# Kernel tuning notes

Hardware: AMD Instinct MI355X
Metric: run time of the kernel (lower is better)

Reference implementation:

```python
import jax, jax.numpy as jnp
import numpy as np

NEG_SLOPE = 0.01  # torch.nn.LeakyReLU default


def setup_inputs() -> dict:
    key = jax.random.key(0)
    ks = jax.random.split(key, 9)
    N_W, N_I, E = 100000, 100000, 2000000
    C_IN, C_OUT, N_CLS = 256, 64, 10
    sc_in = 1.0 / np.sqrt(C_IN)
    sc_cat = 1.0 / np.sqrt(2 * C_OUT)
    return {
        "x_worker": jax.random.normal(ks[0], (N_W, C_IN), dtype=jnp.float32),
        "x_item": jax.random.normal(ks[1], (N_I, C_IN), dtype=jnp.float32),
        "edge_index": jax.random.randint(ks[2], (2, E), 0, N_W, dtype=jnp.int32),
        "W_worker": jax.random.uniform(ks[3], (C_IN, C_OUT), jnp.float32, -sc_in, sc_in),
        "b_worker": jax.random.uniform(ks[4], (C_OUT,), jnp.float32, -sc_in, sc_in),
        "W_item": jax.random.uniform(ks[5], (C_IN, C_OUT), jnp.float32, -sc_in, sc_in),
        "b_item": jax.random.uniform(ks[6], (C_OUT,), jnp.float32, -sc_in, sc_in),
        "W_edge": jax.random.uniform(ks[7], (2 * C_OUT, N_CLS), jnp.float32, -sc_cat, sc_cat),
        "b_edge": jax.random.uniform(ks[8], (N_CLS,), jnp.float32, -sc_cat, sc_cat),
    }


def reference(x_worker, x_item, edge_index, W_worker, b_worker, W_item, b_item, W_edge, b_edge):
    # encoders: Linear + LeakyReLU  -> [N, C_OUT]
    xw = jax.nn.leaky_relu(x_worker @ W_worker + b_worker, NEG_SLOPE)
    xi = jax.nn.leaky_relu(x_item @ W_item + b_item, NEG_SLOPE)
    # gather endpoints per edge and concat -> [E, 2*C_OUT]
    x_cat = jnp.concatenate([xw[edge_index[0]], xi[edge_index[1]]], axis=-1)
    logits = x_cat @ W_edge + b_edge  # [E, num_class]
    return xw, xi, jax.nn.log_softmax(logits, axis=-1)
```

## Files before the change

kernel.cpp:

```cpp
#include <hip/hip_runtime.h>
#include <hip/hip_bf16.h>

#define LOG2E 1.4426950408889634f
#define LN2   0.6931471805599453f

typedef __attribute__((ext_vector_type(8))) short bf16x8;
typedef __attribute__((ext_vector_type(4))) float f32x4;

static __device__ __forceinline__ short f2bf(float f) {
  __hip_bfloat16 h = __float2bfloat16(f);
  return *reinterpret_cast<short*>(&h);
}

static __device__ __forceinline__ void gll16(const float* gsrc, float* ldst) {
  __builtin_amdgcn_global_load_lds(
      (const __attribute__((address_space(1))) void*)gsrc,
      (__attribute__((address_space(3))) void*)ldst, 16, 0, 0);
}

__global__ __launch_bounds__(256) void wprep_kernel(
    const float* __restrict__ Ww, const float* __restrict__ Wi,
    ushort* __restrict__ wfrag)
{
  int id = blockIdx.x * 256 + threadIdx.x;
  if (id >= 4096) return;
  int enc  = id >> 11;
  int f    = (id >> 6) & 31;
  int l    = id & 63;
  int nsub = f >> 3, ks = f & 7;
  const float* __restrict__ W = enc ? Wi : Ww;
  int n  = nsub * 16 + (l & 15);
  int k0 = ks * 32 + (l >> 4) * 8;
  ushort* dst = wfrag + ((size_t)(enc * 32 + f) * 64 + l) * 8;
#pragma unroll
  for (int j = 0; j < 8; ++j)
    dst[j] = (ushort)f2bf(W[(size_t)(k0 + j) * 64 + n]);
}

__global__ __launch_bounds__(256, 2) void enc_mfma4_kernel(
    const float* __restrict__ x0, const float* __restrict__ b0,
    const float* __restrict__ x1, const float* __restrict__ b1,
    const ushort* __restrict__ wfrag, float* __restrict__ out, int M)
{
  __shared__ ushort sfrag[16384];
  __shared__ float  xbuf[2][4096];

  const int enc = blockIdx.y;
  const float* __restrict__ x   = enc ? x1 : x0;
  const float* __restrict__ bia = enc ? b1 : b0;
  float* __restrict__ o = out + (size_t)enc * (size_t)M * 64u;

  const int lane = threadIdx.x & 63;
  const int wid  = threadIdx.x >> 6;
  const int rsel = lane & 15;
  const int kgrp = lane >> 4;
  const int sw   = rsel & 7;

  const int nstrips = (M + 15) >> 4;
  const int bx = blockIdx.x, G = gridDim.x;

  {
    const f32x4* src = (const f32x4*)wfrag + (size_t)enc * 2048;
    f32x4* dst = (f32x4*)sfrag;
#pragma unroll
    for (int i = 0; i < 8; ++i)
      dst[threadIdx.x + 256 * i] = src[threadIdx.x + 256 * i];
  }
  __syncthreads();

  const int niter = (bx < nstrips) ? ((nstrips - 1 - bx) / G + 1) : 0;
  if (niter == 0) return;

  const float bv = bia[wid * 16 + rsel];

  auto stage = [&](int s, int buf) {
#pragma unroll
    for (int j = 0; j < 4; ++j) {
      int R = wid * 4 + j;
      int rg = s * 16 + R; if (rg >= M) rg = M - 1;
      const float* gs = x + (size_t)rg * 256u + ((lane ^ (R & 7)) << 2);
      gll16(gs, &xbuf[buf][R * 256]);
    }
  };

  stage(bx, 0);
  if (niter > 1) {
    stage(bx + G, 1);
    asm volatile("s_waitcnt vmcnt(4)" ::: "memory");
  } else {
    asm volatile("s_waitcnt vmcnt(0)" ::: "memory");
  }
  __builtin_amdgcn_sched_barrier(0);

  for (int i = 0; i < niter; ++i) {
    const int s = bx + i * G;
    if (i) {
      if (i == niter - 1) asm volatile("s_waitcnt vmcnt(4)" ::: "memory");
      else                asm volatile("s_waitcnt vmcnt(8)" ::: "memory");
      __builtin_amdgcn_sched_barrier(0);
    }
    __builtin_amdgcn_s_barrier();
    __builtin_amdgcn_sched_barrier(0);

    const float* xb = xbuf[i & 1];

    bf16x8 a[8];
#pragma unroll
    for (int ks = 0; ks < 8; ++ks) {
      int c0 = ks * 8 + kgrp * 2;
      f32x4 lo = *(const f32x4*)&xb[rsel * 256 + (((c0    ) ^ sw) << 2)];
      f32x4 hi = *(const f32x4*)&xb[rsel * 256 + (((c0 + 1) ^ sw) << 2)];
      a[ks][0] = f2bf(lo.x); a[ks][1] = f2bf(lo.y);
      a[ks][2] = f2bf(lo.z); a[ks][3] = f2bf(lo.w);
      a[ks][4] = f2bf(hi.x); a[ks][5] = f2bf(hi.y);
      a[ks][6] = f2bf(hi.z); a[ks][7] = f2bf(hi.w);
    }

    asm volatile("s_waitcnt lgkmcnt(0)" ::: "memory");
    __builtin_amdgcn_sched_barrier(0);
    __builtin_amdgcn_s_barrier();
    __builtin_amdgcn_sched_barrier(0);

    if (i + 2 < niter) stage(bx + (i + 2) * G, i & 1);

    f32x4 acc = f32x4{0.f, 0.f, 0.f, 0.f};
#pragma unroll
    for (int ks = 0; ks < 8; ++ks) {
      bf16x8 bfr = *(const bf16x8*)(sfrag + ((size_t)((wid * 8 + ks) * 64 + lane)) * 8);
      acc = __builtin_amdgcn_mfma_f32_16x16x32_bf16(a[ks], bfr, acc, 0, 0, 0);
    }

    const int crow = s * 16 + kgrp * 4;
#pragma unroll
    for (int r = 0; r < 4; ++r) {
      int rr = crow + r;
      if (rr < M) {
        float v = acc[r] + bv;
        v = fmaxf(v, 0.01f * v);
        o[(size_t)rr * 64u + wid * 16 + rsel] = v;
      }
    }
  }
}

__global__ __launch_bounds__(256) void proj_kernel(
    const float* __restrict__ feats, const float* __restrict__ W_edge,
    const float* __restrict__ b_edge, float* __restrict__ ws, int M)
{
  const int enc = blockIdx.y;
  int row = blockIdx.x * 256 + threadIdx.x;
  if (row >= M) return;
  const float4* __restrict__ f4 =
      (const float4*)(feats + ((size_t)enc * M + row) * 64u);
  const float* __restrict__ W2 = W_edge + enc * 640;

  float acc[10];
#pragma unroll
  for (int k = 0; k < 10; ++k) acc[k] = enc ? 0.f : b_edge[k];

#pragma unroll 4
  for (int n4 = 0; n4 < 16; ++n4) {
    float4 xv = f4[n4];
    const float* w = W2 + n4 * 40;
#pragma unroll
    for (int k = 0; k < 10; ++k) acc[k] = fmaf(xv.x, w[k],      acc[k]);
#pragma unroll
    for (int k = 0; k < 10; ++k) acc[k] = fmaf(xv.y, w[10 + k], acc[k]);
#pragma unroll
    for (int k = 0; k < 10; ++k) acc[k] = fmaf(xv.z, w[20 + k], acc[k]);
#pragma unroll
    for (int k = 0; k < 10; ++k) acc[k] = fmaf(xv.w, w[30 + k], acc[k]);
  }

  float* orow = ws + ((size_t)enc * M + row) * 16u;
#pragma unroll
  for (int k = 0; k < 10; ++k) orow[k] = acc[k];
}

__global__ __launch_bounds__(256) void edge_kernel(
    const int* __restrict__ ei, const float* __restrict__ ws,
    float* __restrict__ out, int E, int M)
{
  __shared__ float sm[2560];
  long e = (long)blockIdx.x * 256 + threadIdx.x;
  float l[10];
#pragma unroll
  for (int k = 0; k < 10; ++k) l[k] = 0.f;

  if (e < E) {
    int e0 = ei[e];
    int e1 = ei[E + e];
    const float4* pw = (const float4*)ws + (size_t)e0 * 4u;
    const float4* pi = (const float4*)ws + ((size_t)M + e1) * 4u;
    float4 a0 = pw[0], a1 = pw[1], a2 = pw[2];
    float4 c0 = pi[0], c1 = pi[1], c2 = pi[2];
    l[0] = a0.x + c0.x; l[1] = a0.y + c0.y; l[2] = a0.z + c0.z; l[3] = a0.w + c0.w;
    l[4] = a1.x + c1.x; l[5] = a1.y + c1.y; l[6] = a1.z + c1.z; l[7] = a1.w + c1.w;
    l[8] = a2.x + c2.x; l[9] = a2.y + c2.y;
    float m = l[0];
#pragma unroll
    for (int k = 1; k < 10; ++k) m = fmaxf(m, l[k]);
    float s = 0.f;
#pragma unroll
    for (int k = 0; k < 10; ++k) { l[k] = (l[k] - m) * LOG2E; s += exp2f(l[k]); }
    float ls = log2f(s);
#pragma unroll
    for (int k = 0; k < 10; ++k) l[k] = (l[k] - ls) * LN2;
  }

#pragma unroll
  for (int k = 0; k < 10; ++k) sm[threadIdx.x * 10 + k] = l[k];
  __syncthreads();
  const f32x4* sm4 = (const f32x4*)sm;
  f32x4* ob = (f32x4*)(out + (size_t)blockIdx.x * 2560u);
  long lim4 = ((long)E * 10) >> 2;
  long base4 = (long)blockIdx.x * 640;
#pragma unroll
  for (int j = 0; j < 3; ++j) {
    int idx = j * 256 + threadIdx.x;
    if (idx < 640 && base4 + idx < lim4) ob[idx] = sm4[idx];
  }
}

__global__ __launch_bounds__(256) void enc_kernel_f32(
    const float* __restrict__ x0, const float* __restrict__ W0, const float* __restrict__ b0,
    const float* __restrict__ x1, const float* __restrict__ W1, const float* __restrict__ b1,
    float* __restrict__ out, int M)
{
  const int enc = blockIdx.y;
  const float* __restrict__ x = enc ? x1 : x0;
  const float* __restrict__ W = enc ? W1 : W0;
  const float* __restrict__ b = enc ? b1 : b0;
  float* __restrict__ o = out + (size_t)enc * (size_t)M * 64u;

  const int lane = threadIdx.x & 63;
  const int wid  = threadIdx.x >> 6;
  int row0 = __builtin_amdgcn_readfirstlane(blockIdx.x * 64 + wid * 16);
  const float* __restrict__ xrow = x + (size_t)row0 * 256u;

  float acc[16];
#pragma unroll
  for (int r = 0; r < 16; ++r) acc[r] = 0.f;

  if (row0 + 16 <= M) {
#pragma unroll 4
    for (int k = 0; k < 256; ++k) {
      float wv = W[k * 64 + lane];
#pragma unroll
      for (int r = 0; r < 16; ++r)
        acc[r] = fmaf(xrow[r * 256 + k], wv, acc[r]);
    }
    float bias = b[lane];
#pragma unroll
    for (int r = 0; r < 16; ++r) {
      float v = acc[r] + bias;
      v = fmaxf(v, 0.01f * v);
      o[(size_t)(row0 + r) * 64u + lane] = v;
    }
  } else if (row0 < M) {
    int nr = M - row0;
    for (int k = 0; k < 256; ++k) {
      float wv = W[k * 64 + lane];
      for (int r = 0; r < nr; ++r)
        acc[r] = fmaf(xrow[r * 256 + k], wv, acc[r]);
    }
    float bias = b[lane];
    for (int r = 0; r < nr; ++r) {
      float v = acc[r] + bias;
      v = fmaxf(v, 0.01f * v);
      o[(size_t)(row0 + r) * 64u + lane] = v;
    }
  }
}

__global__ __launch_bounds__(256) void edge_kernel_direct(
    const int* __restrict__ ei, const float* __restrict__ feats,
    const float* __restrict__ W_edge, const float* __restrict__ b_edge,
    float* __restrict__ out, int E, int M)
{
  __shared__ float sm[2560];
  long e = (long)blockIdx.x * 256 + threadIdx.x;
  float l[10];
#pragma unroll
  for (int k = 0; k < 10; ++k) l[k] = 0.f;

  if (e < E) {
    int e0 = ei[e];
    int e1 = ei[E + e];
#pragma unroll
    for (int k = 0; k < 10; ++k) l[k] = b_edge[k];
    const float4* fw = (const float4*)(feats + (size_t)e0 * 64u);
    const float4* fi = (const float4*)(feats + ((size_t)M + e1) * 64u);
#pragma unroll 4
    for (int n4 = 0; n4 < 16; ++n4) {
      float4 xv = fw[n4];
      const float* w = W_edge + n4 * 40;
#pragma unroll
      for (int k = 0; k < 10; ++k) l[k] = fmaf(xv.x, w[k],      l[k]);
#pragma unroll
      for (int k = 0; k < 10; ++k) l[k] = fmaf(xv.y, w[10 + k], l[k]);
#pragma unroll
      for (int k = 0; k < 10; ++k) l[k] = fmaf(xv.z, w[20 + k], l[k]);
#pragma unroll
      for (int k = 0; k < 10; ++k) l[k] = fmaf(xv.w, w[30 + k], l[k]);
    }
#pragma unroll 4
    for (int n4 = 0; n4 < 16; ++n4) {
      float4 xv = fi[n4];
      const float* w = W_edge + 640 + n4 * 40;
#pragma unroll
      for (int k = 0; k < 10; ++k) l[k] = fmaf(xv.x, w[k],      l[k]);
#pragma unroll
      for (int k = 0; k < 10; ++k) l[k] = fmaf(xv.y, w[10 + k], l[k]);
#pragma unroll
      for (int k = 0; k < 10; ++k) l[k] = fmaf(xv.z, w[20 + k], l[k]);
#pragma unroll
      for (int k = 0; k < 10; ++k) l[k] = fmaf(xv.w, w[30 + k], l[k]);
    }
    float m = l[0];
#pragma unroll
    for (int k = 1; k < 10; ++k) m = fmaxf(m, l[k]);
    float s = 0.f;
#pragma unroll
    for (int k = 0; k < 10; ++k) { l[k] = (l[k] - m) * LOG2E; s += exp2f(l[k]); }
    float ls = log2f(s);
#pragma unroll
    for (int k = 0; k < 10; ++k) l[k] = (l[k] - ls) * LN2;
  }

#pragma unroll
  for (int k = 0; k < 10; ++k) sm[threadIdx.x * 10 + k] = l[k];
  __syncthreads();
  const f32x4* sm4 = (const f32x4*)sm;
  f32x4* ob = (f32x4*)(out + (size_t)blockIdx.x * 2560u);
  long lim4 = ((long)E * 10) >> 2;
  long base4 = (long)blockIdx.x * 640;
#pragma unroll
  for (int j = 0; j < 3; ++j) {
    int idx = j * 256 + threadIdx.x;
    if (idx < 640 && base4 + idx < lim4) ob[idx] = sm4[idx];
  }
}

extern "C" void kernel_launch(void* const* d_in, const int* in_sizes, int n_in,
                              void* d_out, int out_size, void* d_ws, size_t ws_size,
                              hipStream_t stream)
{
  const float* x_w = (const float*)d_in[0];
  const float* x_i = (const float*)d_in[1];
  const int*   ei  = (const int*)d_in[2];
  const float* W_w = (const float*)d_in[3];
  const float* b_w = (const float*)d_in[4];
  const float* W_i = (const float*)d_in[5];
  const float* b_i = (const float*)d_in[6];
  const float* W_e = (const float*)d_in[7];
  const float* b_e = (const float*)d_in[8];
  float* out = (float*)d_out;

  const int M = in_sizes[0] / 256;
  const int E = in_sizes[2] / 2;

  float* logout = out + (size_t)2 * (size_t)M * 64u;

  const size_t pw_bytes = (size_t)2 * (size_t)M * 16u * sizeof(float);
  const size_t ws_need  = pw_bytes + 65536;

  if (ws_size >= ws_need) {
    float*  ws    = (float*)d_ws;
    ushort* wfrag = (ushort*)((char*)d_ws + pw_bytes);

    wprep_kernel<<<16, 256, 0, stream>>>(W_w, W_i, wfrag);

    dim3 gA(256, 2);
    enc_mfma4_kernel<<<gA, 256, 0, stream>>>(x_w, b_w, x_i, b_i, wfrag, out, M);

    dim3 gB((M + 255) / 256, 2);
    proj_kernel<<<gB, 256, 0, stream>>>(out, W_e, b_e, ws, M);

    dim3 gC((unsigned)((E + 255) / 256));
    edge_kernel<<<gC, 256, 0, stream>>>(ei, ws, logout, E, M);
  } else {
    dim3 gA0((M + 63) / 64, 2);
    enc_kernel_f32<<<gA0, 256, 0, stream>>>(x_w, W_w, b_w, x_i, W_i, b_i, out, M);
    dim3 gC((unsigned)((E + 255) / 256));
    edge_kernel_direct<<<gC, 256, 0, stream>>>(ei, out, W_e, b_e, logout, E, M);
  }
}
```

Baseline: 142.4 us.

## Triple-buffer encoder input tiles and keep weight fragments in registers

The encoder kernel moves from double to triple buffering of the input row tiles, so three strips are in flight. It issues the next prefetch right after the LDS reads, before the bf16 conversion and MFMA. Weight fragments now live in registers instead of LDS, which frees LDS so three blocks can fit per CU, and the grid grows from 256 to 384 blocks per encoder. Row bounds checks are dropped and a host guard sends any M not divisible by 16 to the fallback path. The cost is more register pressure and deeper, hand-counted vmcnt waits that have to stay correct.

```diff
diff --git a/kernel.cpp b/kernel.cpp
--- a/kernel.cpp
+++ b/kernel.cpp
@@ -37,13 +37,12 @@
     dst[j] = (ushort)f2bf(W[(size_t)(k0 + j) * 64 + n]);
 }
 
-__global__ __launch_bounds__(256, 2) void enc_mfma4_kernel(
+__global__ __launch_bounds__(256, 3) void enc_mfma6_kernel(
     const float* __restrict__ x0, const float* __restrict__ b0,
     const float* __restrict__ x1, const float* __restrict__ b1,
     const ushort* __restrict__ wfrag, float* __restrict__ out, int M)
 {
-  __shared__ ushort sfrag[16384];
-  __shared__ float  xbuf[2][4096];
+  __shared__ float xtile[3][4096];
 
   const int enc = blockIdx.y;
   const float* __restrict__ x   = enc ? x1 : x0;
@@ -56,90 +55,91 @@
   const int kgrp = lane >> 4;
   const int sw   = rsel & 7;
 
-  const int nstrips = (M + 15) >> 4;
+  const int nstrips = M >> 4;
   const int bx = blockIdx.x, G = gridDim.x;
-
-  {
-    const f32x4* src = (const f32x4*)wfrag + (size_t)enc * 2048;
-    f32x4* dst = (f32x4*)sfrag;
-#pragma unroll
-    for (int i = 0; i < 8; ++i)
-      dst[threadIdx.x + 256 * i] = src[threadIdx.x + 256 * i];
-  }
-  __syncthreads();
-
   const int niter = (bx < nstrips) ? ((nstrips - 1 - bx) / G + 1) : 0;
   if (niter == 0) return;
 
-  const float bv = bia[wid * 16 + rsel];
+  bf16x8 wf[8];
+#pragma unroll
+  for (int ks = 0; ks < 8; ++ks) {
+    wf[ks] = *(const bf16x8*)(wfrag +
+        ((size_t)((enc * 32 + wid * 8 + ks) * 64 + lane)) * 8);
+    asm volatile("" : "+v"(wf[ks]));
+  }
+  float bv = bia[wid * 16 + rsel];
+  asm volatile("" : "+v"(bv));
 
   auto stage = [&](int s, int buf) {
 #pragma unroll
     for (int j = 0; j < 4; ++j) {
       int R = wid * 4 + j;
-      int rg = s * 16 + R; if (rg >= M) rg = M - 1;
-      const float* gs = x + (size_t)rg * 256u + ((lane ^ (R & 7)) << 2);
-      gll16(gs, &xbuf[buf][R * 256]);
+      const float* gs = x + (size_t)(s * 16 + R) * 256u + ((lane ^ (R & 7)) << 2);
+      gll16(gs, &xtile[buf][R * 256]);
     }
   };
 
   stage(bx, 0);
-  if (niter > 1) {
-    stage(bx + G, 1);
-    asm volatile("s_waitcnt vmcnt(4)" ::: "memory");
-  } else {
-    asm volatile("s_waitcnt vmcnt(0)" ::: "memory");
-  }
+  stage(bx + ((1 < niter) ? 1 : (niter - 1)) * G, 1);
+  stage(bx + ((2 < niter) ? 2 : (niter - 1)) * G, 2);
   __builtin_amdgcn_sched_barrier(0);
 
-  for (int i = 0; i < niter; ++i) {
-    const int s = bx + i * G;
-    if (i) {
-      if (i == niter - 1) asm volatile("s_waitcnt vmcnt(4)" ::: "memory");
-      else                asm volatile("s_waitcnt vmcnt(8)" ::: "memory");
-      __builtin_amdgcn_sched_barrier(0);
-    }
+  for (int k = 0; k < niter; ++k) {
+    if (k == 0)      asm volatile("s_waitcnt vmcnt(8)" ::: "memory");
+    else if (k == 1) asm volatile("s_waitcnt vmcnt(12)" ::: "memory");
+    else             asm volatile("s_waitcnt vmcnt(16)" ::: "memory");
+    __builtin_amdgcn_sched_barrier(0);
     __builtin_amdgcn_s_barrier();
     __builtin_amdgcn_sched_barrier(0);
 
-    const float* xb = xbuf[i & 1];
-
-    bf16x8 a[8];
+    const int b = k % 3;
+    unsigned base = (unsigned)(unsigned long)
+        (__attribute__((address_space(3))) char*)&xtile[b][0];
+    unsigned rowb = base + (unsigned)(rsel << 10);
+
+    f32x4 rv[16];
 #pragma unroll
     for (int ks = 0; ks < 8; ++ks) {
       int c0 = ks * 8 + kgrp * 2;
-      f32x4 lo = *(const f32x4*)&xb[rsel * 256 + (((c0    ) ^ sw) << 2)];
-      f32x4 hi = *(const f32x4*)&xb[rsel * 256 + (((c0 + 1) ^ sw) << 2)];
+      unsigned a0 = rowb + (unsigned)(((c0)     ^ sw) << 4);
+      unsigned a1 = rowb + (unsigned)(((c0 + 1) ^ sw) << 4);
+      asm volatile("ds_read_b128 %0, %1" : "=&v"(rv[2 * ks])     : "v"(a0));
+      asm volatile("ds_read_b128 %0, %1" : "=&v"(rv[2 * ks + 1]) : "v"(a1));
+    }
+    asm volatile("s_waitcnt lgkmcnt(0)" ::: "memory");
+    __builtin_amdgcn_sched_barrier(0);
+    __builtin_amdgcn_s_barrier();
+    __builtin_amdgcn_sched_barrier(0);
+
+    int sn = k + 3; if (sn >= niter) sn = niter - 1;
+    stage(bx + sn * G, b);
+    __builtin_amdgcn_sched_barrier(0);
+
+    bf16x8 a[8];
+#pragma unroll
+    for (int ks = 0; ks < 8; ++ks) {
+      f32x4 lo = rv[2 * ks], hi = rv[2 * ks + 1];
       a[ks][0] = f2bf(lo.x); a[ks][1] = f2bf(lo.y);
       a[ks][2] = f2bf(lo.z); a[ks][3] = f2bf(lo.w);
       a[ks][4] = f2bf(hi.x); a[ks][5] = f2bf(hi.y);
       a[ks][6] = f2bf(hi.z); a[ks][7] = f2bf(hi.w);
     }
 
-    asm volatile("s_waitcnt lgkmcnt(0)" ::: "memory");
-    __builtin_amdgcn_sched_barrier(0);
-    __builtin_amdgcn_s_barrier();
-    __builtin_amdgcn_sched_barrier(0);
-
-    if (i + 2 < niter) stage(bx + (i + 2) * G, i & 1);
-
     f32x4 acc = f32x4{0.f, 0.f, 0.f, 0.f};
 #pragma unroll
-    for (int ks = 0; ks < 8; ++ks) {
-      bf16x8 bfr = *(const bf16x8*)(sfrag + ((size_t)((wid * 8 + ks) * 64 + lane)) * 8);
-      acc = __builtin_amdgcn_mfma_f32_16x16x32_bf16(a[ks], bfr, acc, 0, 0, 0);
-    }
-
+    for (int ks = 0; ks < 8; ++ks)
+      acc = __builtin_amdgcn_mfma_f32_16x16x32_bf16(a[ks], wf[ks], acc, 0, 0, 0);
+
+    const int s = bx + k * G;
     const int crow = s * 16 + kgrp * 4;
+    float* orow = o + (size_t)crow * 64u + wid * 16 + rsel;
 #pragma unroll
     for (int r = 0; r < 4; ++r) {
-      int rr = crow + r;
-      if (rr < M) {
-        float v = acc[r] + bv;
-        v = fmaxf(v, 0.01f * v);
-        o[(size_t)rr * 64u + wid * 16 + rsel] = v;
-      }
-    }
+      float v = acc[r] + bv;
+      v = fmaxf(v, 0.01f * v);
+      orow[r * 64] = v;
+    }
+    __builtin_amdgcn_sched_barrier(0);
   }
 }
 
@@ -365,14 +365,14 @@
   const size_t pw_bytes = (size_t)2 * (size_t)M * 16u * sizeof(float);
   const size_t ws_need  = pw_bytes + 65536;
 
-  if (ws_size >= ws_need) {
+  if (ws_size >= ws_need && (M % 16) == 0) {
     float*  ws    = (float*)d_ws;
     ushort* wfrag = (ushort*)((char*)d_ws + pw_bytes);
 
     wprep_kernel<<<16, 256, 0, stream>>>(W_w, W_i, wfrag);
 
-    dim3 gA(256, 2);
-    enc_mfma4_kernel<<<gA, 256, 0, stream>>>(x_w, b_w, x_i, b_i, wfrag, out, M);
+    dim3 gA(384, 2);
+    enc_mfma6_kernel<<<gA, 256, 0, stream>>>(x_w, b_w, x_i, b_i, wfrag, out, M);
 
     dim3 gB((M + 255) / 256, 2);
     proj_kernel<<<gB, 256, 0, stream>>>(out, W_e, b_e, ws, M);
```

Result: no change. 142.6 us (+0.1%).
